# Optimization experiments

Measured on AMD Instinct MI355X. Metric: run time of the kernel, lower is better.

The kernel has to match this reference:

```python
import jax, jax.numpy as jnp
import numpy as np


def setup_inputs() -> dict:
    key = jax.random.key(0)
    k1, k2 = jax.random.split(key)
    B, S, H, T = 32, 524288, 512, 100
    n_frames = S // H  # 1024
    wrapped_phase = jax.random.uniform(k1, (B, S), dtype=jnp.float32)  # in [0,1)
    tables = jax.random.normal(k2, (B, n_frames + 1, T), dtype=jnp.float32)
    return {"wrapped_phase": wrapped_phase, "tables": tables, "hop_length": H}


def reference(wrapped_phase, tables, hop_length):
    # wrapped_phase: (B, S) in [0,1]; tables: (B, n_frames+1, T); hop_length: python int
    B, S = wrapped_phase.shape
    H = hop_length
    pad = (-S) % H
    wp = jnp.pad(wrapped_phase, ((0, 0), (0, pad)), mode="edge")
    wp = wp.reshape(B, -1, H)          # (B, F, H)
    Fr = wp.shape[1]
    if tables.shape[1] < Fr + 1:
        tables = jnp.pad(tables, ((0, 0), (0, Fr + 1 - tables.shape[1]), (0, 0)), mode="edge")
    else:
        tables = tables[:, : Fr + 1]
    L = tables.shape[2]
    # bilinear interp along table axis
    raw = wp * L                                   # (B, F, H)
    floor = jnp.clip(raw.astype(jnp.int32), 0, L - 1)
    p = raw - floor.astype(wp.dtype)
    # wrap-around pad: append first table entry at the end
    padded = jnp.concatenate([tables, tables[:, :, :1]], axis=2)  # (B, F+1, L+1)
    floor_flow = padded[:, :-1]   # table at frame start
    ceil_flow = padded[:, 1:]     # table at next frame

    def gather(t, idx):
        return jnp.take_along_axis(t, idx, axis=2)  # (B, F, H)

    v_floor = gather(floor_flow, floor) * (1.0 - p) + gather(floor_flow, floor + 1) * p
    v_ceil = gather(ceil_flow, floor) * (1.0 - p) + gather(ceil_flow, floor + 1) * p
    # lerp across hop-time
    p2 = jnp.arange(H, dtype=wp.dtype) / H          # (H,)
    final = v_floor * (1.0 - p2) + v_ceil * p2      # (B, F, H)
    return final.reshape(B, -1)[:, :S]
```

## Files before the change

### kernel.cpp

```cpp
#include <hip/hip_runtime.h>

constexpr int Bc  = 32;
constexpr int Sc  = 524288;
constexpr int Hc  = 512;
constexpr int Tc  = 100;
constexpr int FRc = Sc / Hc;

__global__ __launch_bounds__(128) void gft_kernel(
    const float* __restrict__ wp,
    const float* __restrict__ tables,
    float* __restrict__ out)
{
    __shared__ float shf[Tc + 1];
    __shared__ float shc[Tc + 1];

    const int blk = blockIdx.x;
    const int b   = blk >> 10;
    const int f   = blk & (FRc - 1);
    const int t   = threadIdx.x;

    const float* trow = tables + ((size_t)b * (FRc + 1) + (size_t)f) * Tc;

    for (int i = t; i < 2 * Tc; i += 128) {
        float v = trow[i];
        if (i < Tc) shf[i] = v;
        else        shc[i - Tc] = v;
    }
    if (t == 0) {
        shf[Tc] = trow[0];
        shc[Tc] = trow[Tc];
    }
    __syncthreads();

    const size_t base = (size_t)blk * Hc + (size_t)t * 4;
    const float4 w = *reinterpret_cast<const float4*>(wp + base);

    const float wv[4] = {w.x, w.y, w.z, w.w};
    float r[4];
    #pragma unroll
    for (int j = 0; j < 4; ++j) {
        float raw = wv[j] * (float)Tc;
        int   fl  = (int)raw;
        fl = fl < 0 ? 0 : (fl > Tc - 1 ? Tc - 1 : fl);
        float p   = raw - (float)fl;
        float omp = 1.0f - p;
        float vf  = shf[fl] * omp + shf[fl + 1] * p;
        float vc  = shc[fl] * omp + shc[fl + 1] * p;
        float p2  = (float)(t * 4 + j) * (1.0f / (float)Hc);
        r[j] = vf * (1.0f - p2) + vc * p2;
    }
    *reinterpret_cast<float4*>(out + base) = make_float4(r[0], r[1], r[2], r[3]);
}

extern "C" void kernel_launch(void* const* d_in, const int* in_sizes, int n_in,
                              void* d_out, int out_size, void* d_ws, size_t ws_size,
                              hipStream_t stream) {
    const float* wp     = (const float*)d_in[0];
    const float* tables = (const float*)d_in[1];
    float*       out    = (float*)d_out;
    gft_kernel<<<dim3(Bc * FRc), dim3(128), 0, stream>>>(wp, tables, out);
}
```

Before: 30.35 us.

## Process two frames per block with interleaved float2 tables and nontemporal IO

Each 256-thread block now handles two consecutive frames, so three table rows are shared instead of loading two rows per frame. The floor and ceil tables are interleaved into float2 LDS entries so each tap is a single 8-byte shared load. The phase load is issued before the table fill to overlap global latency with setup. Input loads and output stores use nontemporal hints to avoid polluting cache with streaming data. The trade-off is fewer blocks and a larger shared-memory footprint per block.

```diff
diff --git a/kernel.cpp b/kernel.cpp
--- a/kernel.cpp
+++ b/kernel.cpp
@@ -5,35 +5,41 @@
 constexpr int Hc  = 512;
 constexpr int Tc  = 100;
 constexpr int FRc = Sc / Hc;
+constexpr int FPB = 2;
+constexpr int THREADS = 256;
 
-__global__ __launch_bounds__(128) void gft_kernel(
+typedef float floatx4 __attribute__((ext_vector_type(4)));
+
+__global__ __launch_bounds__(THREADS) void gft_kernel(
     const float* __restrict__ wp,
     const float* __restrict__ tables,
     float* __restrict__ out)
 {
-    __shared__ float shf[Tc + 1];
-    __shared__ float shc[Tc + 1];
+    __shared__ float2 sh[FPB][Tc + 1];
 
     const int blk = blockIdx.x;
-    const int b   = blk >> 10;
-    const int f   = blk & (FRc - 1);
+    const int b   = blk >> 9;
+    const int fp  = blk & 511;
+    const int f   = fp * FPB;
     const int t   = threadIdx.x;
 
+    const size_t base = (size_t)b * Sc + (size_t)fp * (FPB * Hc) + (size_t)t * 4;
+    const floatx4 w = __builtin_nontemporal_load(
+        reinterpret_cast<const floatx4*>(wp + base));
+
     const float* trow = tables + ((size_t)b * (FRc + 1) + (size_t)f) * Tc;
-
-    for (int i = t; i < 2 * Tc; i += 128) {
-        float v = trow[i];
-        if (i < Tc) shf[i] = v;
-        else        shc[i - Tc] = v;
-    }
-    if (t == 0) {
-        shf[Tc] = trow[0];
-        shc[Tc] = trow[Tc];
+    if (t < FPB * (Tc + 1)) {
+        const int fr = t >= (Tc + 1);
+        const int i  = t - fr * (Tc + 1);
+        const int ii = (i == Tc) ? 0 : i;
+        const float x = trow[fr * Tc + ii];
+        const float y = trow[(fr + 1) * Tc + ii];
+        sh[fr][i] = make_float2(x, y);
     }
     __syncthreads();
 
-    const size_t base = (size_t)blk * Hc + (size_t)t * 4;
-    const float4 w = *reinterpret_cast<const float4*>(wp + base);
+    const int fi = t >> 7;
+    const int h0 = (t & 127) * 4;
 
     const float wv[4] = {w.x, w.y, w.z, w.w};
     float r[4];
@@ -44,12 +50,16 @@
         fl = fl < 0 ? 0 : (fl > Tc - 1 ? Tc - 1 : fl);
         float p   = raw - (float)fl;
         float omp = 1.0f - p;
-        float vf  = shf[fl] * omp + shf[fl + 1] * p;
-        float vc  = shc[fl] * omp + shc[fl + 1] * p;
-        float p2  = (float)(t * 4 + j) * (1.0f / (float)Hc);
+        float2 p0 = sh[fi][fl];
+        float2 p1 = sh[fi][fl + 1];
+        float vf  = p0.x * omp + p1.x * p;
+        float vc  = p0.y * omp + p1.y * p;
+        float p2  = (float)(h0 + j) * (1.0f / (float)Hc);
         r[j] = vf * (1.0f - p2) + vc * p2;
     }
-    *reinterpret_cast<float4*>(out + base) = make_float4(r[0], r[1], r[2], r[3]);
+    floatx4 res;
+    res.x = r[0]; res.y = r[1]; res.z = r[2]; res.w = r[3];
+    __builtin_nontemporal_store(res, reinterpret_cast<floatx4*>(out + base));
 }
 
 extern "C" void kernel_launch(void* const* d_in, const int* in_sizes, int n_in,
@@ -58,5 +68,5 @@
     const float* wp     = (const float*)d_in[0];
     const float* tables = (const float*)d_in[1];
     float*       out    = (float*)d_out;
-    gft_kernel<<<dim3(Bc * FRc), dim3(128), 0, stream>>>(wp, tables, out);
+    gft_kernel<<<dim3(Bc * (FRc / FPB)), dim3(THREADS), 0, stream>>>(wp, tables, out);
 }
```

New measurement: 29.58 us. 2.5% less time.
